# Performance work log

Measured on AMD Instinct MI355X. Metric: run time of the kernel, lower is better.

Reference implementation:

```python
import jax, jax.numpy as jnp
import numpy as np
import jax.lax as lax

B, S, E, H = 8, 4096, 1024, 128
TAU = 1.0
MIN_K = 32

def setup_inputs() -> dict:
    key = jax.random.key(0)
    k0, k1, k2, k3 = jax.random.split(key, 4)
    token_embeddings = jax.random.normal(k0, (B, S, E), dtype=jnp.float32)
    w1 = jax.random.normal(k1, (E, H), dtype=jnp.float32) * (1.0 / np.sqrt(E))
    b1 = jnp.zeros((H,), dtype=jnp.float32)
    w2 = jax.random.normal(k2, (H, 1), dtype=jnp.float32) * (1.0 / np.sqrt(H))
    b2 = jnp.zeros((1,), dtype=jnp.float32)
    # uniform noise for Gumbel, same bounds as the original module
    u = jax.random.uniform(k3, (B, S), minval=1e-08, maxval=1.0 - 1e-08, dtype=jnp.float32)
    return {"token_embeddings": token_embeddings, "w1": w1, "b1": b1, "w2": w2, "b2": b2, "u": u}

def reference(token_embeddings, w1, b1, w2, b2, u):
    # scorer MLP: Dense(H) -> relu -> Dense(1), squeeze -> [B, S]
    h = jax.nn.relu(jnp.einsum('bse,eh->bsh', token_embeddings, w1) + b1)
    importance_logits = (jnp.einsum('bsh,ho->bso', h, w2) + b2)[..., 0]  # [B, S]

    # expected_k (value_function is None): soft count of kept tokens
    expected_k = jax.nn.sigmoid(importance_logits).sum(axis=-1)  # [B]
    k = jnp.clip(expected_k.astype(jnp.int32), MIN_K, None)      # [B]

    # Gumbel-softmax top-k, hard=True
    gumbel = -jnp.log(-jnp.log(u))
    soft_mask = jax.nn.softmax((importance_logits + gumbel) / TAU, axis=-1)  # [B, S]

    # hard mask: 1.0 at the top-k[i] positions of soft_mask per row.
    # Equivalent to the original argsort + while_loop scatter: positions with
    # descending-sort rank < k[i] get 1.0.
    order = jnp.argsort(-soft_mask, axis=-1)          # [B, S] descending order
    ranks = jnp.argsort(order, axis=-1)               # rank of each position
    hard_mask = (ranks < k[:, None]).astype(soft_mask.dtype)

    selection_mask = lax.stop_gradient(hard_mask - soft_mask) + soft_mask
    filtered_embeddings = token_embeddings * selection_mask[..., None]
    return filtered_embeddings, selection_mask, expected_k
```

## Files before the change

### kernel.cpp

```cpp
#include <hip/hip_runtime.h>
#include <hip/hip_bf16.h>
#include <math.h>

#define B_ 8
#define S_ 4096
#define E_ 1024
#define H_ 128
#define MIN_K 32
#define OUT_MASK_OFF (B_*S_*E_)
#define OUT_EK_OFF   (B_*S_*E_ + B_*S_)

#define LOGITS_OFF 0
#define SOFT_OFF   131072
#define CNT_OFF    262144
#define KROW_OFF   393216
#define WB_OFF     393248

typedef __attribute__((ext_vector_type(8))) short   frag8;
typedef __attribute__((ext_vector_type(4))) float   fragc;

static __device__ __forceinline__ unsigned short bf16_rne(float f) {
  unsigned u = __float_as_uint(f);
  unsigned r = u + 0x7FFF + ((u >> 16) & 1);
  return (unsigned short)(r >> 16);
}
static __device__ __forceinline__ float bf16_to_f32(unsigned short h) {
  return __uint_as_float(((unsigned)h) << 16);
}

__global__ __launch_bounds__(256) void prep_w_kernel(
    const float* __restrict__ w1, unsigned short* __restrict__ wb)
{
  int id = blockIdx.x * 256 + threadIdx.x;
  int k  = id >> 5;
  int n4 = id & 31;
  float4 w = *(const float4*)(w1 + k * H_ + n4 * 4);
  int t  = k >> 5;
  int kp = k & 31;
#pragma unroll
  for (int e = 0; e < 4; ++e) {
    float f = (e == 0) ? w.x : (e == 1) ? w.y : (e == 2) ? w.z : w.w;
    unsigned short hi = bf16_rne(f);
    unsigned short lo = bf16_rne(f - bf16_to_f32(hi));
    int n = n4 * 4 + e;
    wb[t * 8192 +        n * 32 + kp] = hi;
    wb[t * 8192 + 4096 + n * 32 + kp] = lo;
  }
}

#define KT 32
#define NTILES (E_ / KT)
#define AS 36
#define XS 40

#define ISSUE_LOADS(Sa0, Sa1, Sq0, Sq1, T)                  \
    Sa0 = *(const float4*)(xsrc + (T) * KT);                \
    Sa1 = *(const float4*)(xsrc + (T) * KT + 4);            \
    Sq0 = *(const uint4*)(bsrc + (T) * 8192);               \
    Sq1 = *(const uint4*)(bsrc + (T) * 8192 + 8);

#define WRITE_STAGE(BUF, Sa0, Sa1, Sq0, Sq1) {              \
    *(float4*)&as_f[BUF][aoff]     = Sa0;                   \
    *(float4*)&as_f[BUF][aoff + 4] = Sa1;                   \
    unsigned short* bd_ = bplane ? &bs_lo[BUF][boff]        \
                                 : &bs_hi[BUF][boff];       \
    *(uint4*)(bd_)     = Sq0;                               \
    *(uint4*)(bd_ + 8) = Sq1; }

#define COMPUTE(BUF) {                                                        \
    frag8 ah[2], al[2], bh[4], bl[4];                                         \
    _Pragma("unroll") for (int mt = 0; mt < 2; ++mt) {                        \
      int a_ = (mg * 32 + mt * 16 + l15) * AS + quad * 8;                     \
      float4 f0_ = *(const float4*)&as_f[BUF][a_];                            \
      float4 f1_ = *(const float4*)&as_f[BUF][a_ + 4];                        \
      float ff_[8] = {f0_.x, f0_.y, f0_.z, f0_.w, f1_.x, f1_.y, f1_.z, f1_.w};\
      _Pragma("unroll") for (int e = 0; e < 8; ++e) {                         \
        unsigned short hi_ = bf16_rne(ff_[e]);                                \
        ah[mt][e] = (short)hi_;                                               \
        al[mt][e] = (short)bf16_rne(ff_[e] - bf16_to_f32(hi_)); } }           \
    _Pragma("unroll") for (int nt = 0; nt < 4; ++nt) {                        \
      int a_ = (ng * 64 + nt * 16 + l15) * XS + quad * 8;                     \
      bh[nt] = *(const frag8*)&bs_hi[BUF][a_];                                \
      bl[nt] = *(const frag8*)&bs_lo[BUF][a_]; }                              \
    _Pragma("unroll") for (int mt = 0; mt < 2; ++mt)                          \
      _Pragma("unroll") for (int nt = 0; nt < 4; ++nt) {                      \
        acc[mt][nt] = __builtin_amdgcn_mfma_f32_16x16x32_bf16(ah[mt], bh[nt], acc[mt][nt], 0, 0, 0); \
        acc[mt][nt] = __builtin_amdgcn_mfma_f32_16x16x32_bf16(ah[mt], bl[nt], acc[mt][nt], 0, 0, 0); \
        acc[mt][nt] = __builtin_amdgcn_mfma_f32_16x16x32_bf16(al[mt], bh[nt], acc[mt][nt], 0, 0, 0); } }

__global__ __launch_bounds__(512, 2) void scorer_kernel(
    const float* __restrict__ x,
    const unsigned short* __restrict__ wb,
    const float* __restrict__ b1, const float* __restrict__ w2,
    const float* __restrict__ b2, float* __restrict__ logits)
{
  __shared__ float          as_f[2][128 * AS];
  __shared__ unsigned short bs_hi[2][128 * XS];
  __shared__ unsigned short bs_lo[2][128 * XS];
  __shared__ float part[2][128];

  const int tid  = threadIdx.x;
  const int wv   = tid >> 6;
  const int lane = tid & 63;
  const int l15  = lane & 15;
  const int quad = lane >> 4;
  const int mg   = wv >> 1;
  const int ng   = wv & 1;
  const int m0   = blockIdx.x * 128;

  const int r = tid >> 2, p = tid & 3;
  const float* __restrict__ xsrc = x + (size_t)(m0 + r) * E_ + p * 8;
  const unsigned short* __restrict__ bsrc = wb + tid * 16;
  const int bplane = tid >> 8;
  const int boff   = ((tid >> 1) & 127) * XS + (tid & 1) * 16;
  const int aoff   = r * AS + p * 8;

  fragc acc[2][4];
#pragma unroll
  for (int mt = 0; mt < 2; ++mt)
#pragma unroll
    for (int nt = 0; nt < 4; ++nt)
      acc[mt][nt] = (fragc)(0.f);

  float4 a0_S0, a1_S0; uint4 q0_S0, q1_S0;
  float4 a0_S1, a1_S1; uint4 q0_S1, q1_S1;

  ISSUE_LOADS(a0_S0, a1_S0, q0_S0, q1_S0, 0)
  ISSUE_LOADS(a0_S1, a1_S1, q0_S1, q1_S1, 1)
  WRITE_STAGE(0, a0_S0, a1_S0, q0_S0, q1_S0)
  __syncthreads();

  for (int tp = 0; tp < 16; ++tp) {
    const bool more = (tp < 15);
    if (more) { ISSUE_LOADS(a0_S0, a1_S0, q0_S0, q1_S0, 2 * tp + 2) }
    __builtin_amdgcn_sched_barrier(0);
    COMPUTE(0)
    WRITE_STAGE(1, a0_S1, a1_S1, q0_S1, q1_S1)
    __syncthreads();
    if (more) { ISSUE_LOADS(a0_S1, a1_S1, q0_S1, q1_S1, 2 * tp + 3) }
    __builtin_amdgcn_sched_barrier(0);
    COMPUTE(1)
    if (more) { WRITE_STAGE(0, a0_S0, a1_S0, q0_S0, q1_S0) }
    __syncthreads();
  }

  float b1v[4], w2v[4];
#pragma unroll
  for (int nt = 0; nt < 4; ++nt) {
    int n = ng * 64 + nt * 16 + l15;
    b1v[nt] = b1[n]; w2v[nt] = w2[n];
  }
  float v[2][4];
#pragma unroll
  for (int mt = 0; mt < 2; ++mt)
#pragma unroll
    for (int reg = 0; reg < 4; ++reg) {
      float pacc = 0.f;
#pragma unroll
      for (int nt = 0; nt < 4; ++nt) {
        float h = acc[mt][nt][reg] + b1v[nt];
        h = h > 0.f ? h : 0.f;
        pacc = fmaf(h, w2v[nt], pacc);
      }
      v[mt][reg] = pacc;
    }
#pragma unroll
  for (int mask = 1; mask < 16; mask <<= 1)
#pragma unroll
    for (int mt = 0; mt < 2; ++mt)
#pragma unroll
      for (int reg = 0; reg < 4; ++reg)
        v[mt][reg] += __shfl_xor(v[mt][reg], mask);

  if (l15 == 0) {
#pragma unroll
    for (int mt = 0; mt < 2; ++mt)
#pragma unroll
      for (int reg = 0; reg < 4; ++reg)
        part[ng][mg * 32 + mt * 16 + quad * 4 + reg] = v[mt][reg];
  }
  __syncthreads();
  if (tid < 128)
    logits[m0 + tid] = (part[0][tid] + part[1][tid]) + b2[0];
}

__global__ __launch_bounds__(1024) void row_kernel(
    const float* __restrict__ logits, const float* __restrict__ u,
    float* __restrict__ soft, int* __restrict__ krow, float* __restrict__ ek_out)
{
  const int b = blockIdx.x;
  const int t = threadIdx.x;
  const float* Lrow = logits + b * S_;
  const float* urow = u + b * S_;

  __shared__ double red[1024];
  __shared__ float  redf[1024];

  float z[4];
  double psig = 0.0;
  float zmax = -INFINITY;
#pragma unroll
  for (int i = 0; i < 4; ++i) {
    int j = t + i * 1024;
    float L = Lrow[j];
    float g = -logf(-logf(urow[j]));
    z[i] = L + g;
    psig += (double)(1.f / (1.f + expf(-L)));
    zmax = fmaxf(zmax, z[i]);
  }
  red[t] = psig; redf[t] = zmax;
  __syncthreads();
  for (int s2 = 512; s2 > 0; s2 >>= 1) {
    if (t < s2) { red[t] += red[t + s2]; redf[t] = fmaxf(redf[t], redf[t + s2]); }
    __syncthreads();
  }
  __shared__ float m_sh; __shared__ double ek_sh;
  if (t == 0) { m_sh = redf[0]; ek_sh = red[0]; }
  __syncthreads();
  float m = m_sh;

  float e[4];
  double pexp = 0.0;
#pragma unroll
  for (int i = 0; i < 4; ++i) { e[i] = expf(z[i] - m); pexp += (double)e[i]; }
  red[t] = pexp;
  __syncthreads();
  for (int s2 = 512; s2 > 0; s2 >>= 1) {
    if (t < s2) red[t] += red[t + s2];
    __syncthreads();
  }
  __shared__ float den_sh;
  if (t == 0) den_sh = (float)red[0];
  __syncthreads();
  float den = den_sh;
#pragma unroll
  for (int i = 0; i < 4; ++i) soft[b * S_ + t + i * 1024] = e[i] / den;

  if (t == 0) {
    float ekf = (float)ek_sh;
    int k = (int)ekf;
    if (k < MIN_K) k = MIN_K;
    krow[b] = k;
    ek_out[b] = ekf;
  }
}

__global__ __launch_bounds__(256) void rank_kernel(
    const float* __restrict__ soft, int* __restrict__ counts)
{
  __shared__ float4 sjs[256];
  const int b  = blockIdx.z;
  const int ic = blockIdx.x;
  const int jc = blockIdx.y;
  const int tid = threadIdx.x;
  const float* row = soft + b * S_;

  sjs[tid] = ((const float4*)row)[jc * 256 + tid];
  const int i = ic * 256 + tid;
  const float si = row[i];
  __syncthreads();

  int cnt = 0;
  const int jbase = jc * 1024;
  for (int j4 = 0; j4 < 256; ++j4) {
    float4 vv = sjs[j4];
    int j = jbase + j4 * 4;
    cnt += (vv.x > si) || (vv.x == si && (j + 0) < i);
    cnt += (vv.y > si) || (vv.y == si && (j + 1) < i);
    cnt += (vv.z > si) || (vv.z == si && (j + 2) < i);
    cnt += (vv.w > si) || (vv.w == si && (j + 3) < i);
  }
  atomicAdd(&counts[b * S_ + i], cnt);
}

__global__ __launch_bounds__(256) void filter_kernel(
    const float* __restrict__ x, const float* __restrict__ soft,
    const int* __restrict__ counts, const int* __restrict__ krow,
    float* __restrict__ out, float* __restrict__ mask_out)
{
  const int token = blockIdx.x;
  const int b = token >> 12;
  const float s = soft[token];
  const float h = (counts[token] < krow[b]) ? 1.f : 0.f;
  const float sel = (h - s) + s;

  size_t base = (size_t)token * (E_ / 4) + threadIdx.x;
  float4 v = ((const float4*)x)[base];
  v.x *= sel; v.y *= sel; v.z *= sel; v.w *= sel;
  ((float4*)out)[base] = v;
  if (threadIdx.x == 0) mask_out[token] = sel;
}

extern "C" void kernel_launch(void* const* d_in, const int* in_sizes, int n_in,
                              void* d_out, int out_size, void* d_ws, size_t ws_size,
                              hipStream_t stream) {
  const float* x  = (const float*)d_in[0];
  const float* w1 = (const float*)d_in[1];
  const float* b1 = (const float*)d_in[2];
  const float* w2 = (const float*)d_in[3];
  const float* b2 = (const float*)d_in[4];
  const float* u  = (const float*)d_in[5];

  float* out = (float*)d_out;
  float* out_filt = out;
  float* out_mask = out + OUT_MASK_OFF;
  float* out_ek   = out + OUT_EK_OFF;

  char* ws = (char*)d_ws;
  float*          ws_logits = (float*)(ws + LOGITS_OFF);
  float*          ws_soft   = (float*)(ws + SOFT_OFF);
  int*            ws_cnt    = (int*)(ws + CNT_OFF);
  int*            ws_krow   = (int*)(ws + KROW_OFF);
  unsigned short* ws_wb     = (unsigned short*)(ws + WB_OFF);

  hipMemsetAsync(ws_cnt, 0, B_ * S_ * sizeof(int), stream);
  prep_w_kernel<<<dim3(128), dim3(256), 0, stream>>>(w1, ws_wb);
  scorer_kernel<<<dim3(B_ * S_ / 128), dim3(512), 0, stream>>>(
      x, ws_wb, b1, w2, b2, ws_logits);
  row_kernel<<<dim3(B_), dim3(1024), 0, stream>>>(ws_logits, u, ws_soft, ws_krow, out_ek);
  rank_kernel<<<dim3(16, 4, 8), dim3(256), 0, stream>>>(ws_soft, ws_cnt);
  filter_kernel<<<dim3(B_ * S_), dim3(256), 0, stream>>>(
      x, ws_soft, ws_cnt, ws_krow, out_filt, out_mask);
}
```

Baseline: 311.6 us.

## Restructure scorer GEMM to per-wave 16-row tiles with direct global B loads

The scorer kernel now gives each wavefront its own 16 rows across the full 128-wide hidden dimension. The split-W1 fragments are read straight from global memory (L2/L1) instead of being staged through shared memory. This removes the block-wide __syncthreads and the B tiles in LDS, and each wave stages only its own A rows. The cost is that W1 is re-read by every wave rather than shared inside the block, which adds cache traffic. There are also twice as many smaller blocks.

```diff
diff --git a/kernel.cpp b/kernel.cpp
--- a/kernel.cpp
+++ b/kernel.cpp
@@ -51,137 +51,113 @@
 #define KT 32
 #define NTILES (E_ / KT)
 #define AS 36
-#define XS 40
-
-#define ISSUE_LOADS(Sa0, Sa1, Sq0, Sq1, T)                  \
-    Sa0 = *(const float4*)(xsrc + (T) * KT);                \
-    Sa1 = *(const float4*)(xsrc + (T) * KT + 4);            \
-    Sq0 = *(const uint4*)(bsrc + (T) * 8192);               \
-    Sq1 = *(const uint4*)(bsrc + (T) * 8192 + 8);
-
-#define WRITE_STAGE(BUF, Sa0, Sa1, Sq0, Sq1) {              \
-    *(float4*)&as_f[BUF][aoff]     = Sa0;                   \
-    *(float4*)&as_f[BUF][aoff + 4] = Sa1;                   \
-    unsigned short* bd_ = bplane ? &bs_lo[BUF][boff]        \
-                                 : &bs_hi[BUF][boff];       \
-    *(uint4*)(bd_)     = Sq0;                               \
-    *(uint4*)(bd_ + 8) = Sq1; }
-
-#define COMPUTE(BUF) {                                                        \
-    frag8 ah[2], al[2], bh[4], bl[4];                                         \
-    _Pragma("unroll") for (int mt = 0; mt < 2; ++mt) {                        \
-      int a_ = (mg * 32 + mt * 16 + l15) * AS + quad * 8;                     \
-      float4 f0_ = *(const float4*)&as_f[BUF][a_];                            \
-      float4 f1_ = *(const float4*)&as_f[BUF][a_ + 4];                        \
-      float ff_[8] = {f0_.x, f0_.y, f0_.z, f0_.w, f1_.x, f1_.y, f1_.z, f1_.w};\
-      _Pragma("unroll") for (int e = 0; e < 8; ++e) {                         \
-        unsigned short hi_ = bf16_rne(ff_[e]);                                \
-        ah[mt][e] = (short)hi_;                                               \
-        al[mt][e] = (short)bf16_rne(ff_[e] - bf16_to_f32(hi_)); } }           \
-    _Pragma("unroll") for (int nt = 0; nt < 4; ++nt) {                        \
-      int a_ = (ng * 64 + nt * 16 + l15) * XS + quad * 8;                     \
-      bh[nt] = *(const frag8*)&bs_hi[BUF][a_];                                \
-      bl[nt] = *(const frag8*)&bs_lo[BUF][a_]; }                              \
-    _Pragma("unroll") for (int mt = 0; mt < 2; ++mt)                          \
-      _Pragma("unroll") for (int nt = 0; nt < 4; ++nt) {                      \
-        acc[mt][nt] = __builtin_amdgcn_mfma_f32_16x16x32_bf16(ah[mt], bh[nt], acc[mt][nt], 0, 0, 0); \
-        acc[mt][nt] = __builtin_amdgcn_mfma_f32_16x16x32_bf16(ah[mt], bl[nt], acc[mt][nt], 0, 0, 0); \
-        acc[mt][nt] = __builtin_amdgcn_mfma_f32_16x16x32_bf16(al[mt], bh[nt], acc[mt][nt], 0, 0, 0); } }
-
-__global__ __launch_bounds__(512, 2) void scorer_kernel(
+
+__global__ __launch_bounds__(256, 2) void scorer_kernel(
     const float* __restrict__ x,
     const unsigned short* __restrict__ wb,
     const float* __restrict__ b1, const float* __restrict__ w2,
     const float* __restrict__ b2, float* __restrict__ logits)
 {
-  __shared__ float          as_f[2][128 * AS];
-  __shared__ unsigned short bs_hi[2][128 * XS];
-  __shared__ unsigned short bs_lo[2][128 * XS];
-  __shared__ float part[2][128];
+  __shared__ float as_f[2][4][16 * AS];
 
   const int tid  = threadIdx.x;
   const int wv   = tid >> 6;
   const int lane = tid & 63;
   const int l15  = lane & 15;
   const int quad = lane >> 4;
-  const int mg   = wv >> 1;
-  const int ng   = wv & 1;
-  const int m0   = blockIdx.x * 128;
-
-  const int r = tid >> 2, p = tid & 3;
+  const int m0   = blockIdx.x * 64 + wv * 16;
+
+  const int r = lane >> 2, p = lane & 3;
   const float* __restrict__ xsrc = x + (size_t)(m0 + r) * E_ + p * 8;
-  const unsigned short* __restrict__ bsrc = wb + tid * 16;
-  const int bplane = tid >> 8;
-  const int boff   = ((tid >> 1) & 127) * XS + (tid & 1) * 16;
-  const int aoff   = r * AS + p * 8;
-
-  fragc acc[2][4];
-#pragma unroll
-  for (int mt = 0; mt < 2; ++mt)
-#pragma unroll
-    for (int nt = 0; nt < 4; ++nt)
-      acc[mt][nt] = (fragc)(0.f);
-
-  float4 a0_S0, a1_S0; uint4 q0_S0, q1_S0;
-  float4 a0_S1, a1_S1; uint4 q0_S1, q1_S1;
-
-  ISSUE_LOADS(a0_S0, a1_S0, q0_S0, q1_S0, 0)
-  ISSUE_LOADS(a0_S1, a1_S1, q0_S1, q1_S1, 1)
-  WRITE_STAGE(0, a0_S0, a1_S0, q0_S0, q1_S0)
-  __syncthreads();
-
+  const int aoff = r * AS + p * 8;
+  const int foff = l15 * AS + quad * 8;
+
+  const unsigned short* __restrict__ bb = wb + l15 * 32 + quad * 8;
+
+  fragc acc[8];
+#pragma unroll
+  for (int nt = 0; nt < 8; ++nt) acc[nt] = (fragc)(0.f);
+
+  float4 a0_S0, a1_S0, a0_S1, a1_S1;
+
+#define A_COMPUTE_STEP(BUF, T) {                                              \
+    float4 f0_ = *(const float4*)&as_f[BUF][wv][foff];                        \
+    float4 f1_ = *(const float4*)&as_f[BUF][wv][foff + 4];                    \
+    frag8 ah, al;                                                             \
+    { float ff_[8] = {f0_.x, f0_.y, f0_.z, f0_.w, f1_.x, f1_.y, f1_.z, f1_.w};\
+      _Pragma("unroll") for (int e = 0; e < 8; ++e) {                         \
+        unsigned short hi_ = bf16_rne(ff_[e]);                                \
+        ah[e] = (short)hi_;                                                   \
+        al[e] = (short)bf16_rne(ff_[e] - bf16_to_f32(hi_)); } }               \
+    const unsigned short* bth_ = bb + (T) * 8192;                             \
+    const unsigned short* btl_ = bth_ + 4096;                                 \
+    _Pragma("unroll") for (int nt = 0; nt < 8; ++nt) {                        \
+      frag8 bh_ = *(const frag8*)(bth_ + nt * 512);                           \
+      frag8 bl_ = *(const frag8*)(btl_ + nt * 512);                           \
+      acc[nt] = __builtin_amdgcn_mfma_f32_16x16x32_bf16(ah, bh_, acc[nt], 0, 0, 0); \
+      acc[nt] = __builtin_amdgcn_mfma_f32_16x16x32_bf16(ah, bl_, acc[nt], 0, 0, 0); \
+      acc[nt] = __builtin_amdgcn_mfma_f32_16x16x32_bf16(al, bh_, acc[nt], 0, 0, 0); } }
+
+  a0_S0 = *(const float4*)(xsrc);          a1_S0 = *(const float4*)(xsrc + 4);
+  a0_S1 = *(const float4*)(xsrc + KT);     a1_S1 = *(const float4*)(xsrc + KT + 4);
+  *(float4*)&as_f[0][wv][aoff] = a0_S0;    *(float4*)&as_f[0][wv][aoff + 4] = a1_S0;
+
+#pragma unroll 1
   for (int tp = 0; tp < 16; ++tp) {
-    const bool more = (tp < 15);
-    if (more) { ISSUE_LOADS(a0_S0, a1_S0, q0_S0, q1_S0, 2 * tp + 2) }
-    __builtin_amdgcn_sched_barrier(0);
-    COMPUTE(0)
-    WRITE_STAGE(1, a0_S1, a1_S1, q0_S1, q1_S1)
-    __syncthreads();
-    if (more) { ISSUE_LOADS(a0_S1, a1_S1, q0_S1, q1_S1, 2 * tp + 3) }
-    __builtin_amdgcn_sched_barrier(0);
-    COMPUTE(1)
-    if (more) { WRITE_STAGE(0, a0_S0, a1_S0, q0_S0, q1_S0) }
-    __syncthreads();
-  }
-
-  float b1v[4], w2v[4];
-#pragma unroll
-  for (int nt = 0; nt < 4; ++nt) {
-    int n = ng * 64 + nt * 16 + l15;
-    b1v[nt] = b1[n]; w2v[nt] = w2[n];
-  }
-  float v[2][4];
-#pragma unroll
-  for (int mt = 0; mt < 2; ++mt)
-#pragma unroll
-    for (int reg = 0; reg < 4; ++reg) {
-      float pacc = 0.f;
-#pragma unroll
-      for (int nt = 0; nt < 4; ++nt) {
-        float h = acc[mt][nt][reg] + b1v[nt];
-        h = h > 0.f ? h : 0.f;
-        pacc = fmaf(h, w2v[nt], pacc);
+    {
+      const int t = 2 * tp;
+      if (t + 2 < NTILES) {
+        a0_S0 = *(const float4*)(xsrc + (t + 2) * KT);
+        a1_S0 = *(const float4*)(xsrc + (t + 2) * KT + 4);
       }
-      v[mt][reg] = pacc;
+      A_COMPUTE_STEP(0, t)
+      *(float4*)&as_f[1][wv][aoff] = a0_S1;
+      *(float4*)&as_f[1][wv][aoff + 4] = a1_S1;
     }
+    {
+      const int t = 2 * tp + 1;
+      if (t + 2 < NTILES) {
+        a0_S1 = *(const float4*)(xsrc + (t + 2) * KT);
+        a1_S1 = *(const float4*)(xsrc + (t + 2) * KT + 4);
+      }
+      A_COMPUTE_STEP(1, t)
+      if (tp < 15) {
+        *(float4*)&as_f[0][wv][aoff] = a0_S0;
+        *(float4*)&as_f[0][wv][aoff + 4] = a1_S0;
+      }
+    }
+  }
+
+  float b1v[8], w2v[8];
+#pragma unroll
+  for (int nt = 0; nt < 8; ++nt) {
+    b1v[nt] = b1[nt * 16 + l15];
+    w2v[nt] = w2[nt * 16 + l15];
+  }
+  float pv[4];
+#pragma unroll
+  for (int reg = 0; reg < 4; ++reg) {
+    float pacc = 0.f;
+#pragma unroll
+    for (int nt = 0; nt < 8; ++nt) {
+      float h = acc[nt][reg] + b1v[nt];
+      h = h > 0.f ? h : 0.f;
+      pacc = fmaf(h, w2v[nt], pacc);
+    }
+    pv[reg] = pacc;
+  }
 #pragma unroll
   for (int mask = 1; mask < 16; mask <<= 1)
 #pragma unroll
-    for (int mt = 0; mt < 2; ++mt)
-#pragma unroll
-      for (int reg = 0; reg < 4; ++reg)
-        v[mt][reg] += __shfl_xor(v[mt][reg], mask);
+    for (int reg = 0; reg < 4; ++reg)
+      pv[reg] += __shfl_xor(pv[reg], mask);
 
   if (l15 == 0) {
 #pragma unroll
-    for (int mt = 0; mt < 2; ++mt)
-#pragma unroll
-      for (int reg = 0; reg < 4; ++reg)
-        part[ng][mg * 32 + mt * 16 + quad * 4 + reg] = v[mt][reg];
-  }
-  __syncthreads();
-  if (tid < 128)
-    logits[m0 + tid] = (part[0][tid] + part[1][tid]) + b2[0];
+    for (int reg = 0; reg < 4; ++reg)
+      logits[m0 + quad * 4 + reg] = pv[reg] + b2[0];
+  }
+#undef A_COMPUTE_STEP
 }
 
 __global__ __launch_bounds__(1024) void row_kernel(
@@ -315,7 +291,7 @@
 
   hipMemsetAsync(ws_cnt, 0, B_ * S_ * sizeof(int), stream);
   prep_w_kernel<<<dim3(128), dim3(256), 0, stream>>>(w1, ws_wb);
-  scorer_kernel<<<dim3(B_ * S_ / 128), dim3(512), 0, stream>>>(
+  scorer_kernel<<<dim3(B_ * S_ / 64), dim3(256), 0, stream>>>(
       x, ws_wb, b1, w2, b2, ws_logits);
   row_kernel<<<dim3(B_), dim3(1024), 0, stream>>>(ws_logits, u, ws_soft, ws_krow, out_ek);
   rank_kernel<<<dim3(16, 4, 8), dim3(256), 0, stream>>>(ws_soft, ws_cnt);
```

New measurement: 354.6 us. 13.8% more time.
